# Performance work log

Measured on AMD Instinct MI355X. Metric: run time of the kernel, lower is better.

## Reference

```python
import jax, jax.numpy as jnp
import numpy as np

V, D, H, B, S, T, N_EXTRA = 32000, 256, 512, 16, 400, 100, 50


def _lstm_cell(x, h, c, Wih, Whh, b):
    g = x @ Wih.T + h @ Whh.T + b
    i, f, gg, o = jnp.split(g, 4, axis=-1)
    c = jax.nn.sigmoid(f) * c + jax.nn.sigmoid(i) * jnp.tanh(gg)
    h = jax.nn.sigmoid(o) * jnp.tanh(c)
    return h, c


def _run_lstm(xs, m, Wih, Whh, b):
    # xs: [S,B,D], m: [S,B,1] validity mask (packed-sequence semantics)
    Bz, Hh = xs.shape[1], Whh.shape[1]
    init = (jnp.zeros((Bz, Hh), xs.dtype), jnp.zeros((Bz, Hh), xs.dtype))
    def step(carry, inp):
        h, c = carry
        x, mm = inp
        hn, cn = _lstm_cell(x, h, c, Wih, Whh, b)
        h = jnp.where(mm, hn, h)
        c = jnp.where(mm, cn, c)
        return (h, c), jnp.where(mm, hn, 0.0)
    (h, c), ys = jax.lax.scan(step, init, (xs, m))
    return ys, h, c


def setup_inputs():
    key = jax.random.key(0)
    ks = jax.random.split(key, 20)
    def gn(k, shape, scale=0.05):
        return jax.random.normal(k, shape, dtype=jnp.float32) * scale
    inp = {}
    inp["source"] = jax.random.randint(ks[0], (B, S), 0, V)
    inp["source_extended"] = jax.random.randint(ks[1], (B, S), 0, V + N_EXTRA)
    inp["source_length"] = jax.random.randint(ks[2], (B,), S // 2, S + 1)
    inp["target"] = jax.random.randint(ks[3], (B, T), 0, V)
    inp["emb"] = gn(ks[4], (V, D), 0.1)
    inp["enc_Wih_f"] = gn(ks[5], (4 * H, D))
    inp["enc_Whh_f"] = gn(ks[6], (4 * H, H))
    inp["enc_b_f"] = jnp.zeros((4 * H,), jnp.float32)
    inp["enc_Wih_b"] = gn(ks[7], (4 * H, D))
    inp["enc_Whh_b"] = gn(ks[8], (4 * H, H))
    inp["enc_b_b"] = jnp.zeros((4 * H,), jnp.float32)
    inp["Wproj"] = gn(ks[9], (H, 2 * H))
    inp["bproj"] = jnp.zeros((H,), jnp.float32)
    inp["W2h"] = gn(ks[10], (H, 2 * H))
    inp["b2h"] = jnp.zeros((H,), jnp.float32)
    inp["W2c"] = gn(ks[11], (H, 2 * H))
    inp["b2c"] = jnp.zeros((H,), jnp.float32)
    inp["Wo1"] = gn(ks[12], (H, 2 * H))
    inp["bo1"] = jnp.zeros((H,), jnp.float32)
    inp["Wo2"] = gn(ks[13], (D, H))
    inp["dec_Wih"] = gn(ks[14], (4 * H, 2 * D))
    inp["dec_Whh"] = gn(ks[15], (4 * H, H))
    inp["dec_b"] = jnp.zeros((4 * H,), jnp.float32)
    inp["Wpgen"] = gn(ks[16], (1, 2 * H + 2 * D))
    inp["bpgen"] = jnp.zeros((1,), jnp.float32)
    return inp


def reference(source, source_extended, source_length, target, emb,
              enc_Wih_f, enc_Whh_f, enc_b_f, enc_Wih_b, enc_Whh_b, enc_b_b,
              Wproj, bproj, W2h, b2h, W2c, b2c, Wo1, bo1, Wo2,
              dec_Wih, dec_Whh, dec_b, Wpgen, bpgen):
    mask = jnp.arange(S)[None, :] < source_length[:, None]  # [B,S]
    w_s = emb[source]                                        # [B,S,D]
    xs = jnp.swapaxes(w_s, 0, 1)                             # [S,B,D]
    m = jnp.swapaxes(mask, 0, 1)[:, :, None]                 # [S,B,1]
    # bidirectional LSTM encoder
    ys_f, h_f, c_f = _run_lstm(xs, m, enc_Wih_f, enc_Whh_f, enc_b_f)
    ys_b, h_b, c_b = _run_lstm(xs[::-1], m[::-1], enc_Wih_b, enc_Whh_b, enc_b_b)
    ys_b = ys_b[::-1]
    enc_outs = jnp.swapaxes(jnp.concatenate([ys_f, ys_b], -1), 0, 1)  # [B,S,2H]
    enc_outs = enc_outs @ Wproj.T + bproj                             # [B,S,H]
    dec_h = jnp.concatenate([h_f, h_b], -1) @ W2h.T + b2h             # [B,H]
    dec_c = jnp.concatenate([c_f, c_b], -1) @ W2c.T + b2c             # [B,H]
    lens = source_length[:, None].astype(enc_outs.dtype)
    seq_mean = (enc_outs * mask[..., None]).sum(1) / lens             # [B,H]
    def out_proj(x):
        return jnp.tanh(x @ Wo1.T + bo1) @ Wo2.T
    dec_out0 = out_proj(jnp.concatenate([dec_h, seq_mean], -1))       # [B,D]
    neg = jnp.finfo(enc_outs.dtype).min
    extra = jnp.zeros((B, N_EXTRA), enc_outs.dtype)
    rows = jnp.arange(B)[:, None]
    w_t = jnp.swapaxes(emb[target], 0, 1)                             # [T,B,D]
    def step(carry, x_t):
        dec_out, h, c = carry
        x = jnp.concatenate([x_t, dec_out], -1)                       # [B,2D]
        h, c = _lstm_cell(x, h, c, dec_Wih, dec_Whh, dec_b)
        scores = jnp.einsum('bh,bsh->bs', h, enc_outs)
        attn = jax.nn.softmax(jnp.where(mask, scores, neg), axis=-1)  # point_dist
        context = jnp.einsum('bs,bsh->bh', attn, enc_outs)
        p_gen = jax.nn.sigmoid(jnp.concatenate([context, h, x], -1) @ Wpgen.T + bpgen)  # [B,1]
        dec_out = out_proj(jnp.concatenate([h, context], -1))         # [B,D]
        logit = dec_out @ emb.T                                       # [B,V]
        vocab_dist = jnp.concatenate([p_gen * jax.nn.softmax(logit, axis=-1), extra], -1)
        final = vocab_dist.at[rows, source_extended].add((1.0 - p_gen) * attn) + 1e-20
        return (dec_out, h, c), jnp.log(final)
    _, logits = jax.lax.scan(step, (dec_out0, dec_h, dec_c), w_t)
    return logits  # [T,B,V+N_EXTRA]
```

## Files before the change

### kernel.cpp

```cpp
#include <hip/hip_runtime.h>

#define V_SZ 32000
#define D_SZ 256
#define H_SZ 512
#define B_SZ 16
#define S_SZ 400
#define T_SZ 100
#define G4   2048
#define VX   32050
#define LINE 32

typedef unsigned short ushort_t;
typedef __attribute__((ext_vector_type(8))) __bf16 bf16x8;
typedef __attribute__((ext_vector_type(8))) unsigned short ushort8_t;
typedef __attribute__((ext_vector_type(4))) float f32x4;

__device__ __forceinline__ ushort_t f2bf(float x) {
  union { float f; unsigned u; } v; v.f = x;
  unsigned r = v.u + 0x7fffu + ((v.u >> 16) & 1u);
  return (ushort_t)(r >> 16);
}
__device__ __forceinline__ float bf2f(ushort_t x) {
  union { unsigned u; float f; } v; v.u = ((unsigned)x) << 16; return v.f;
}
__device__ __forceinline__ float bfu2f(unsigned x) {
  union { unsigned u; float f; } v; v.u = x << 16; return v.f;
}
__device__ __forceinline__ float sigf(float x) { return 1.0f / (1.0f + __expf(-x)); }
__device__ __forceinline__ float tanh_f(float x) {
  float e = __expf(2.0f * x);
  return 1.0f - 2.0f / (e + 1.0f);
}
__device__ __forceinline__ float dot4(f32x4 a, f32x4 b) {
  return a.x * b.x + a.y * b.y + a.z * b.z + a.w * b.w;
}
__device__ __forceinline__ void stg(float* p, float v) {
  __hip_atomic_store(p, v, __ATOMIC_RELAXED, __HIP_MEMORY_SCOPE_AGENT);
}
__device__ __forceinline__ void stg_u32(unsigned* p, unsigned v) {
  __hip_atomic_store(p, v, __ATOMIC_RELAXED, __HIP_MEMORY_SCOPE_AGENT);
}

__device__ __forceinline__ void slot_barrier(unsigned* slots, int myslot, int nslots,
                                             unsigned pc) {
  asm volatile("s_waitcnt vmcnt(0)" ::: "memory");
  __syncthreads();
  if (threadIdx.x == 0)
    __hip_atomic_store(&slots[myslot * LINE], pc, __ATOMIC_RELAXED, __HIP_MEMORY_SCOPE_AGENT);
  if (threadIdx.x < 64) {
    const int i0 = threadIdx.x, i1 = threadIdx.x + 64;
    for (;;) {
      unsigned v0 = pc, v1 = pc;
      if (i0 < nslots)
        v0 = __hip_atomic_load(&slots[i0 * LINE], __ATOMIC_RELAXED, __HIP_MEMORY_SCOPE_AGENT);
      if (i1 < nslots)
        v1 = __hip_atomic_load(&slots[i1 * LINE], __ATOMIC_RELAXED, __HIP_MEMORY_SCOPE_AGENT);
      if (__all((v0 >= pc) & (v1 >= pc))) break;
      __builtin_amdgcn_s_sleep(1);
    }
  }
  __syncthreads();
}

__global__ __launch_bounds__(256) void cvt_kernel(const float* in, ushort_t* outp, int n) {
  int i = blockIdx.x * 256 + threadIdx.x;
  int stride = gridDim.x * 256;
  for (; i < n; i += stride) outp[i] = f2bf(in[i]);
}

__global__ __launch_bounds__(256) void cvt_strided_kernel(const float* in, ushort_t* outp) {
  int gid = blockIdx.x * 256 + threadIdx.x;
  int r = gid >> 8, d = gid & 255;
  outp[gid] = f2bf(in[(size_t)r * 512 + d]);
}

__global__ __launch_bounds__(256) void cvt_wo2t_kernel(const float* wo2, ushort_t* outp) {
  int gid = blockIdx.x * 256 + threadIdx.x;
  int h = gid >> 8, d = gid & 255;
  outp[gid] = f2bf(wo2[(size_t)d * 512 + h]);
}

__global__ __launch_bounds__(256) void wfused_kernel(const float* dwih, const float* wo2,
                                                     float* wf) {
  __shared__ float xr_s[256];
  int r = blockIdx.x;
  xr_s[threadIdx.x] = dwih[(size_t)r * 512 + 256 + threadIdx.x];
  __syncthreads();
  float a0 = 0, a1 = 0;
  for (int d = 0; d < 256; ++d) {
    float x = xr_s[d];
    a0 += x * wo2[(size_t)d * 512 + threadIdx.x];
    a1 += x * wo2[(size_t)d * 512 + threadIdx.x + 256];
  }
  wf[(size_t)r * 512 + threadIdx.x] = a0;
  wf[(size_t)r * 512 + threadIdx.x + 256] = a1;
}

__global__ __launch_bounds__(256) void wfp_kernel(const float* wpgen, const float* wo2,
                                                  float* wfp) {
  int h = blockIdx.x * 256 + threadIdx.x;
  float a = 0;
  for (int d = 0; d < 256; ++d) a += wpgen[1280 + d] * wo2[(size_t)d * 512 + h];
  wfp[h] = a;
}

__global__ __launch_bounds__(256) void pack_whh_kernel(const float* whh_f, const float* whh_b,
                                                       ushort_t* outp) {
  int gid = blockIdx.x * 256 + threadIdx.x;
  int col = gid & 511;
  int p_g = gid >> 9;
  int dir = p_g >> 11, p = p_g & 2047;
  int ub = p >> 6, g = (p >> 4) & 3, u = p & 15;
  const float* src = dir ? whh_b : whh_f;
  outp[gid] = f2bf(src[(size_t)(g * 512 + ub * 16 + u) * 512 + col]);
}

__global__ __launch_bounds__(256) void pack_wdec_kernel(const float* dwhh, const float* wfused,
                                                        ushort_t* outp) {
  int gid = blockIdx.x * 256 + threadIdx.x;
  int col = gid & 1023;
  int p = gid >> 10;
  int ub = p >> 4, g = (p >> 2) & 3, u = p & 3;
  int row = g * 512 + ub * 4 + u;
  float v = (col < 512) ? dwhh[(size_t)row * 512 + col] : wfused[(size_t)row * 512 + (col - 512)];
  outp[gid] = f2bf(v);
}

__global__ __launch_bounds__(256) void gxT_kernel(const float* gx, float* gxT) {
  int t = blockIdx.y;
  int r = blockIdx.x * 256 + threadIdx.x;
  float v[16];
#pragma unroll
  for (int b = 0; b < 16; ++b) v[b] = gx[((size_t)t * 16 + b) * G4 + r];
  f32x4* dst = (f32x4*)(gxT + ((size_t)t * G4 + r) * 16);
#pragma unroll
  for (int q = 0; q < 4; ++q) {
    f32x4 w = {v[q * 4], v[q * 4 + 1], v[q * 4 + 2], v[q * 4 + 3]};
    dst[q] = w;
  }
}

__global__ __launch_bounds__(256) void gather_src_kernel(const ushort_t* emb_bf, const int* source,
                                                         ushort_t* xs_bf) {
  int gid = blockIdx.x * 256 + threadIdx.x;
  int r = gid >> 5, e = gid & 31;
  int s = r >> 4, b = r & 15;
  int tok = source[b * S_SZ + s];
  ((ushort8_t*)xs_bf)[gid] = ((const ushort8_t*)emb_bf)[(size_t)tok * 32 + e];
}
__global__ __launch_bounds__(256) void gather_tgt_kernel(const ushort_t* emb_bf, const int* target,
                                                         ushort_t* xt_bf) {
  int gid = blockIdx.x * 256 + threadIdx.x;
  int r = gid >> 5, e = gid & 31;
  int t = r >> 4, b = r & 15;
  int tok = target[b * T_SZ + t];
  ((ushort8_t*)xt_bf)[gid] = ((const ushort8_t*)emb_bf)[(size_t)tok * 32 + e];
}

__device__ __forceinline__ void mfma_16x64(const ushort_t* A, const ushort_t* B_, int K,
                                           int m0, int n0, f32x4 acc[4]) {
  const int lane = threadIdx.x & 63;
  const int lr = lane & 15, kh = lane >> 4;
  const ushort_t* ap = A + (size_t)(m0 + lr) * K + kh * 8;
  const ushort_t* bp = B_ + (size_t)(n0 + lr) * K + kh * 8;
  for (int k0 = 0; k0 < K; k0 += 32) {
    bf16x8 av = *(const bf16x8*)(ap + k0);
#pragma unroll
    for (int s = 0; s < 4; ++s) {
      bf16x8 bv = *(const bf16x8*)(bp + (size_t)s * 16 * K + k0);
      acc[s] = __builtin_amdgcn_mfma_f32_16x16x32_bf16(av, bv, acc[s], 0, 0, 0);
    }
  }
}

__global__ __launch_bounds__(256) void gemm_abt_bias(const ushort_t* A, const ushort_t* Bm,
                                                     const float* bias, float* out, int K) {
  int wave = threadIdx.x >> 6;
  int m0 = blockIdx.y * 16;
  int n0 = blockIdx.x * 256 + wave * 64;
  f32x4 acc[4] = {};
  mfma_16x64(A, Bm, K, m0, n0, acc);
  int lane = threadIdx.x & 63, lr = lane & 15, kh = lane >> 4;
#pragma unroll
  for (int s = 0; s < 4; ++s) {
    int n = n0 + s * 16 + lr;
    float bv = bias[n];
#pragma unroll
    for (int i = 0; i < 4; ++i) {
      int m = m0 + kh * 4 + i;
      out[(size_t)m * G4 + n] = acc[s][i] + bv;
    }
  }
}

__global__ __launch_bounds__(256) void gemm_encout(const ushort_t* ys_cat, const ushort_t* wproj_bf,
                                                   const float* bproj, float* enc_outs) {
  int wave = threadIdx.x >> 6;
  int m0 = blockIdx.y * 16;
  int n0 = blockIdx.x * 256 + wave * 64;
  f32x4 acc[4] = {};
  mfma_16x64(ys_cat, wproj_bf, 2 * H_SZ, m0, n0, acc);
  int lane = threadIdx.x & 63, lr = lane & 15, kh = lane >> 4;
#pragma unroll
  for (int s = 0; s < 4; ++s) {
    int n = n0 + s * 16 + lr;
    float bv = bproj[n];
#pragma unroll
    for (int i = 0; i < 4; ++i) {
      int m = m0 + kh * 4 + i;
      int b = m & 15, si = m >> 4;
      enc_outs[((size_t)b * S_SZ + si) * H_SZ + n] = acc[s][i] + bv;
    }
  }
}

__global__ __launch_bounds__(256) void gemm_e2(const ushort_t* emb_bf, const ushort_t* wo2t_bf,
                                               ushort_t* e2) {
  int wave = threadIdx.x >> 6;
  int m0 = blockIdx.y * 16;
  int n0 = blockIdx.x * 256 + wave * 64;
  f32x4 acc[4] = {};
  mfma_16x64(emb_bf, wo2t_bf, 256, m0, n0, acc);
  int lane = threadIdx.x & 63, lr = lane & 15, kh = lane >> 4;
#pragma unroll
  for (int s = 0; s < 4; ++s) {
    int n = n0 + s * 16 + lr;
#pragma unroll
    for (int i = 0; i < 4; ++i) {
      int m = m0 + kh * 4 + i;
      e2[(size_t)m * 512 + n] = f2bf(acc[s][i]);
    }
  }
}

__global__ __launch_bounds__(256) void gemm_logits(const ushort_t* tmp_bf, const ushort_t* e2_bf,
                                                   float* out) {
  int wave = threadIdx.x >> 6;
  int m0 = blockIdx.x * 16;
  int n0 = blockIdx.y * 256 + wave * 64;
  f32x4 acc[4] = {};
  mfma_16x64(tmp_bf, e2_bf, 512, m0, n0, acc);
  int lane = threadIdx.x & 63, lr = lane & 15, kh = lane >> 4;
#pragma unroll
  for (int s = 0; s < 4; ++s) {
    int n = n0 + s * 16 + lr;
#pragma unroll
    for (int i = 0; i < 4; ++i) {
      int m = m0 + kh * 4 + i;
      out[(size_t)m * VX + n] = acc[s][i];
    }
  }
}

__global__ __launch_bounds__(256) void enc_kernel(const float* gx_f, const float* gx_b,
                                                  const ushort_t* whh_pk, const int* src_len,
                                                  unsigned* hbf_f, unsigned* hbf_b,
                                                  unsigned* ys_cat_u32, float* h_final,
                                                  float* c_final, unsigned* ctrs) {
  __shared__ float gates_s[4 * 16 * 17];
  const int blk = blockIdx.x, tid = threadIdx.x;
  const int dir = blk >> 5, ub = blk & 31, j0 = ub * 16;
  const int g = tid >> 6, lane = tid & 63, lr = lane & 15, kh = lane >> 4;
  const float* gx = dir ? gx_b : gx_f;
  unsigned* hb = dir ? hbf_b : hbf_f;
  unsigned* slots = ctrs + dir * 1024;
  const ushort_t* wrow =
      whh_pk + (size_t)(((dir * 32 + ub) * 4 + g) * 16 + lr) * 512 + kh * 8;
  const int bc = tid >> 4, uc = tid & 15;
  const int len_b = src_len[bc];
  float c_reg = 0.0f, h_reg = 0.0f;

  int maxlen;
  {
    int v = src_len[lane & 15];
    v = max(v, __shfl_xor(v, 1));
    v = max(v, __shfl_xor(v, 2));
    v = max(v, __shfl_xor(v, 4));
    v = max(v, __shfl_xor(v, 8));
    maxlen = v;
  }
  for (int i = tid; i < (S_SZ - maxlen) * 128; i += 256) {
    int s = maxlen + (i >> 7);
    int r = i & 127;
    int bb = r >> 3, k = r & 7;
    ys_cat_u32[(size_t)(s * 16 + bb) * 512 + dir * 256 + (j0 >> 1) + k] = 0u;
  }

  float gxa[4];
  {
    const int s0 = dir ? (maxlen - 1) : 0;
    const float* g0 = gx + (size_t)s0 * (16 * 2048) + g * 512 + j0 + lr;
#pragma unroll
    for (int i = 0; i < 4; ++i) gxa[i] = g0[(size_t)(kh * 4 + i) * 2048];
  }

  for (int t = 0; t < maxlen; ++t) {
    const int s_pos = dir ? (maxlen - 1 - t) : t;
    float gxn[4] = {0.f, 0.f, 0.f, 0.f};
    if (t + 1 < maxlen) {
      const int sn = dir ? (maxlen - 2 - t) : (t + 1);
      const float* gn = gx + (size_t)sn * (16 * 2048) + g * 512 + j0 + lr;
#pragma unroll
      for (int i = 0; i < 4; ++i) gxn[i] = gn[(size_t)(kh * 4 + i) * 2048];
    }
    f32x4 acc = {0.f, 0.f, 0.f, 0.f};
    const ushort_t* ap = (const ushort_t*)(hb + (size_t)t * 4096) + lr * 512 + kh * 8;
#pragma unroll
    for (int k0 = 0; k0 < 512; k0 += 32)
      acc = __builtin_amdgcn_mfma_f32_16x16x32_bf16(*(const bf16x8*)(ap + k0),
                                                    *(const bf16x8*)(wrow + k0), acc, 0, 0, 0);
#pragma unroll
    for (int i = 0; i < 4; ++i)
      gates_s[(g * 16 + lr) * 17 + kh * 4 + i] = acc[i] + gxa[i];
    __syncthreads();
    float gi = gates_s[uc * 17 + bc];
    float gf = gates_s[(16 + uc) * 17 + bc];
    float gg = gates_s[(32 + uc) * 17 + bc];
    float go = gates_s[(48 + uc) * 17 + bc];
    bool msk = s_pos < len_b;
    float cn = sigf(gf) * c_reg + sigf(gi) * tanh_f(gg);
    float hn = sigf(go) * tanh_f(cn);
    float hout = msk ? hn : h_reg;
    if (msk) c_reg = cn;
    h_reg = hout;
    unsigned hbits = (unsigned)f2bf(hout);
    unsigned hpart = __shfl_xor(hbits, 1);
    unsigned ybits = msk ? (unsigned)f2bf(hn) : 0u;
    unsigned ypart = __shfl_xor(ybits, 1);
    if ((uc & 1) == 0) {
      stg_u32(&hb[(size_t)(t + 1) * 4096 + bc * 256 + ((j0 + uc) >> 1)], hbits | (hpart << 16));
      ys_cat_u32[(size_t)(s_pos * 16 + bc) * 512 + dir * 256 + ((j0 + uc) >> 1)] =
          ybits | (ypart << 16);
    }
    if (t == maxlen - 1) {
      h_final[dir * 8192 + bc * 512 + j0 + uc] = hout;
      c_final[dir * 8192 + bc * 512 + j0 + uc] = c_reg;
    }
    if (t + 1 < maxlen) slot_barrier(slots, ub, 32, (unsigned)(t + 1));
#pragma unroll
    for (int i = 0; i < 4; ++i) gxa[i] = gxn[i];
  }
}

__global__ __launch_bounds__(256) void seqmean_kernel(const float* enc_outs, const int* src_len,
                                                      float* seq_mean) {
  int b = blockIdx.x >> 1;
  int j = (blockIdx.x & 1) * 256 + threadIdx.x;
  int L = src_len[b];
  float a = 0;
  for (int s = 0; s < L; ++s) a += enc_outs[((size_t)b * S_SZ + s) * H_SZ + j];
  seq_mean[b * 512 + j] = a / (float)L;
}

__global__ __launch_bounds__(256) void init_state_kernel(const float* h_final, const float* c_final,
                                                         const float* w2h, const float* b2h,
                                                         const float* w2c, const float* b2c,
                                                         unsigned* h_u32, float* c_init) {
  int gid = blockIdx.x * 256 + threadIdx.x;
  int half = gid >> 13;
  int idx = gid & 8191;
  int b = idx >> 9, j = idx & 511;
  const float* src = half ? c_final : h_final;
  const float* w = (half ? w2c : w2h) + (size_t)j * 1024;
  float acc = (half ? b2c : b2h)[j];
  const f32x4* s0 = (const f32x4*)(src + b * 512);
  const f32x4* s1 = (const f32x4*)(src + 8192 + b * 512);
  const f32x4* w0 = (const f32x4*)w;
  const f32x4* w1 = w0 + 128;
  float a = 0;
  for (int k = 0; k < 128; ++k) a += dot4(s0[k], w0[k]);
  for (int k = 0; k < 128; ++k) a += dot4(s1[k], w1[k]);
  acc += a;
  if (half) {
    c_init[idx] = acc;
  } else {
    unsigned bits = (unsigned)f2bf(acc);
    unsigned pb2 = __shfl_xor(bits, 1);
    if ((j & 1) == 0) h_u32[b * 256 + (j >> 1)] = bits | (pb2 << 16);
  }
}

__global__ __launch_bounds__(256) void tmp0_kernel(const unsigned* h0_u32, const float* seq_mean,
                                                   const float* wo1, const float* bo1,
                                                   unsigned* tmp_u32) {
  int gid = blockIdx.x * 256 + threadIdx.x;
  int b = gid >> 9, j = gid & 511;
  const f32x4* x1 = (const f32x4*)(seq_mean + b * 512);
  const f32x4* w0 = (const f32x4*)(wo1 + (size_t)j * 1024);
  const f32x4* w1 = w0 + 128;
  float a = bo1[j];
  float p = 0;
  const ushort_t* h0 = (const ushort_t*)(h0_u32) + b * 512;
  for (int k = 0; k < 128; ++k) {
    f32x4 hv = {bf2f(h0[k * 4]), bf2f(h0[k * 4 + 1]), bf2f(h0[k * 4 + 2]), bf2f(h0[k * 4 + 3])};
    p += dot4(hv, w0[k]);
  }
  for (int k = 0; k < 128; ++k) p += dot4(x1[k], w1[k]);
  float tv = tanh_f(a + p);
  unsigned bits = (unsigned)f2bf(tv);
  unsigned pb2 = __shfl_xor(bits, 1);
  if ((j & 1) == 0) tmp_u32[b * 256 + (j >> 1)] = bits | (pb2 << 16);
}

__global__ __launch_bounds__(256) void dec_kernel(
    const ushort_t* xt_bf, const int* src_len, const ushort_t* wdec_pk,
    const float* wpgen, const float* bpgen, const float* wfp, const ushort_t* wo1_bf,
    const float* bo1, const float* enc_outs, const float* gxT, unsigned* h_u32,
    const float* c_init, unsigned* tmp_u32, float* ctx_part, float* z_part, float* zinv,
    float* pgen_o, float* pexp, unsigned* ctrs) {
  __shared__ ushort_t ec_s[50 * 512];
  __shared__ float part_s[4 * 16 * 17];
  __shared__ f32x4 smem4[272];
  __shared__ float red_s[8];
  __shared__ float p_s[64];
  float* sm = (float*)smem4;
  unsigned* gslots = ctrs + 2048;

  const int blk = blockIdx.x, tid = threadIdx.x;
  const int w = tid >> 6, lane = tid & 63, lr = lane & 15, kh = lane >> 4;
  const int j0 = blk * 4;
  const ushort_t* wrow = wdec_pk + (size_t)(blk * 16 + lr) * 1024 + w * 256 + kh * 8;
  const int b_c = (tid >> 2) & 15, u_c = tid & 3;
  float c_reg = (tid < 64) ? c_init[b_c * 512 + j0 + u_c] : 0.0f;
  const int b_pb = blk >> 3, ch = blk & 7, s0c = ch * 50;
  const int len_pb = src_len[b_pb];
  const int nc = ch;
  unsigned* grslots = ctrs + 8192 + b_pb * 256;
  unsigned gpc = 0;

  {
    const f32x4* ebase = (const f32x4*)(enc_outs + ((size_t)b_pb * S_SZ + s0c) * H_SZ);
    unsigned* dst = (unsigned*)ec_s;
    for (int i = tid; i < 6400; i += 256) {
      f32x4 v = ebase[i];
      dst[2 * i] = (unsigned)f2bf(v.x) | ((unsigned)f2bf(v.y) << 16);
      dst[2 * i + 1] = (unsigned)f2bf(v.z) | ((unsigned)f2bf(v.w) << 16);
    }
  }

  float gxa[4] = {0.f, 0.f, 0.f, 0.f};
  if (tid < 64) {
#pragma unroll
    for (int g2 = 0; g2 < 4; ++g2)
      gxa[g2] = gxT[((size_t)(g2 * 512 + j0 + u_c)) * 16 + b_c];
  }

  for (int t = 0; t < T_SZ; ++t) {
    {
      f32x4 acc = {0.f, 0.f, 0.f, 0.f};
      const unsigned* asrc = (w < 2) ? (h_u32 + (size_t)t * 4096) : (tmp_u32 + (size_t)t * 4096);
      const ushort_t* ap = (const ushort_t*)asrc + lr * 512 + (w & 1) * 256 + kh * 8;
#pragma unroll
      for (int k0 = 0; k0 < 256; k0 += 32)
        acc = __builtin_amdgcn_mfma_f32_16x16x32_bf16(*(const bf16x8*)(ap + k0),
                                                      *(const bf16x8*)(wrow + k0), acc, 0, 0, 0);
#pragma unroll
      for (int i = 0; i < 4; ++i) part_s[(w * 16 + lr) * 17 + kh * 4 + i] = acc[i];
      __syncthreads();
      if (tid < 64) {
        float gt[4];
#pragma unroll
        for (int g2 = 0; g2 < 4; ++g2) {
          int p = g2 * 4 + u_c;
          float a = gxa[g2];
#pragma unroll
          for (int w2 = 0; w2 < 4; ++w2) a += part_s[(w2 * 16 + p) * 17 + b_c];
          gt[g2] = a;
        }
        float cn = sigf(gt[1]) * c_reg + sigf(gt[0]) * tanh_f(gt[2]);
        c_reg = cn;
        float hn = sigf(gt[3]) * tanh_f(cn);
        unsigned bits = (unsigned)f2bf(hn);
        unsigned pb2 = __shfl_xor(bits, 1);
        if ((u_c & 1) == 0)
          stg_u32(&h_u32[(size_t)(t + 1) * 4096 + b_c * 256 + ((j0 + u_c) >> 1)],
                  bits | (pb2 << 16));
      }
    }
    slot_barrier(gslots, blk, 128, ++gpc);
    {
      if (tid < 64 && t + 1 < T_SZ) {
#pragma unroll
        for (int g2 = 0; g2 < 4; ++g2)
          gxa[g2] = gxT[((size_t)(t + 1) * G4 + g2 * 512 + j0 + u_c) * 16 + b_c];
      }
      if (tid < 128) {
        unsigned v0 = h_u32[(size_t)(t + 1) * 4096 + b_pb * 256 + tid * 2];
        unsigned v1 = h_u32[(size_t)(t + 1) * 4096 + b_pb * 256 + tid * 2 + 1];
        f32x4 hv = {bfu2f(v0 & 0xffffu), bfu2f(v0 >> 16), bfu2f(v1 & 0xffffu), bfu2f(v1 >> 16)};
        ((f32x4*)sm)[tid] = hv;
      }
      __syncthreads();
      int st = tid >> 2, kq = tid & 3;
      if (st < 50) {
        const ushort8_t* er = (const ushort8_t*)(ec_s + st * 512) + kq * 16;
        const f32x4* hr = (const f32x4*)sm + kq * 32;
        float sc = 0;
#pragma unroll 4
        for (int k = 0; k < 16; ++k) {
          ushort8_t w8 = er[k];
          f32x4 w0 = {bf2f(w8[0]), bf2f(w8[1]), bf2f(w8[2]), bf2f(w8[3])};
          f32x4 w1 = {bf2f(w8[4]), bf2f(w8[5]), bf2f(w8[6]), bf2f(w8[7])};
          sc += dot4(hr[2 * k], w0) + dot4(hr[2 * k + 1], w1);
        }
        sc += __shfl_xor(sc, 1);
        sc += __shfl_xor(sc, 2);
        if (kq == 0) {
          int s_abs = s0c + st;
          float p = (s_abs < len_pb) ? __expf(sc) : 0.0f;
          p_s[st] = p;
          pexp[((size_t)t * 16 + b_pb) * S_SZ + s_abs] = p;
        }
      }
      __syncthreads();
      if (tid == 0) {
        float z = 0;
        for (int s = 0; s < 50; ++s) z += p_s[s];
        stg(&z_part[((size_t)t * 16 + b_pb) * 8 + ch], z);
      }
      float a0 = 0, a1 = 0;
      for (int s = 0; s < 50; ++s) {
        float p = p_s[s];
        a0 += p * bf2f(ec_s[s * 512 + tid]);
        a1 += p * bf2f(ec_s[s * 512 + tid + 256]);
      }
      float* cp = ctx_part + (((size_t)t * 16 + b_pb) * 8 + ch) * 512;
      stg(&cp[tid], a0);
      stg(&cp[tid + 256], a1);
    }
    slot_barrier(grslots, ch, 8, (unsigned)(t + 1));
    {
      float* h_s = sm;
      float* ctx_s = sm + 512;
      const float* zp = z_part + ((size_t)t * 16 + b_pb) * 8;
      float z = 0;
#pragma unroll
      for (int c2 = 0; c2 < 8; ++c2) z += zp[c2];
      float inv = 1.0f / z;
      const float* cpb = ctx_part + ((size_t)t * 16 + b_pb) * 8 * 512;
      float c0 = 0, c1 = 0;
#pragma unroll
      for (int c2 = 0; c2 < 8; ++c2) {
        c0 += cpb[c2 * 512 + tid];
        c1 += cpb[c2 * 512 + tid + 256];
      }
      ctx_s[tid] = c0 * inv;
      ctx_s[tid + 256] = c1 * inv;
      __syncthreads();
      const ushort_t* tmpp = (const ushort_t*)(tmp_u32 + (size_t)t * 4096) + b_pb * 512;
      float tp0 = bf2f(tmpp[tid]);
      float tp1 = bf2f(tmpp[tid + 256]);
      float xe = bf2f(xt_bf[((size_t)t * 16 + b_pb) * 256 + tid]);
      float pg = wpgen[tid] * ctx_s[tid] + wpgen[tid + 256] * ctx_s[tid + 256] +
                 wpgen[512 + tid] * h_s[tid] + wpgen[512 + tid + 256] * h_s[tid + 256] +
                 wpgen[1024 + tid] * xe + wfp[tid] * tp0 + wfp[tid + 256] * tp1;
#pragma unroll
      for (int o = 32; o; o >>= 1) pg += __shfl_xor(pg, o);
      if (lane == 0) red_s[w] = pg;
      __syncthreads();
      if (nc == 0 && tid == 0) {
        pgen_o[t * 16 + b_pb] = sigf(red_s[0] + red_s[1] + red_s[2] + red_s[3] + bpgen[0]);
        zinv[t * 16 + b_pb] = inv;
      }
      int nidx = tid >> 2, kq = tid & 3;
      int n = nc * 64 + nidx;
      const ushort8_t* wrp = (const ushort8_t*)(wo1_bf + (size_t)n * 1024) + kq * 32;
      const f32x4* xr2 =
          (kq < 2) ? ((const f32x4*)h_s + kq * 64) : ((const f32x4*)ctx_s + (kq - 2) * 64);
      float a = 0;
#pragma unroll 4
      for (int k = 0; k < 32; ++k) {
        ushort8_t w8 = wrp[k];
        f32x4 w0 = {bf2f(w8[0]), bf2f(w8[1]), bf2f(w8[2]), bf2f(w8[3])};
        f32x4 w1 = {bf2f(w8[4]), bf2f(w8[5]), bf2f(w8[6]), bf2f(w8[7])};
        a += dot4(xr2[2 * k], w0) + dot4(xr2[2 * k + 1], w1);
      }
      a += __shfl_xor(a, 1);
      a += __shfl_xor(a, 2);
      float tv = tanh_f(a + bo1[n]);
      unsigned bits = (unsigned)f2bf(tv);
      unsigned pbits = __shfl_xor(bits, 4);
      if (kq == 0 && (nidx & 1) == 0)
        stg_u32(&tmp_u32[(size_t)(t + 1) * 4096 + b_pb * 256 + ((nc * 64 + nidx) >> 1)],
                bits | (pbits << 16));
    }
    if (t + 1 < T_SZ) slot_barrier(gslots, blk, 128, ++gpc);
  }
}

__global__ __launch_bounds__(1024) void finalize_kernel(float* out, const float* pexp,
                                                        const float* zinv, const float* pgen_i,
                                                        const int* src_ext) {
  __shared__ float scat[VX];
  __shared__ float red[64];
  const int row = blockIdx.x;
  const int b = row & 15;
  const int tid = threadIdx.x;
  for (int i = tid; i < VX; i += 1024) scat[i] = 0.0f;
  __syncthreads();
  const float pg = pgen_i[row];
  const float inv = zinv[row];
  if (tid < S_SZ) {
    float v = (1.0f - pg) * pexp[(size_t)row * S_SZ + tid] * inv;
    int col = src_ext[b * S_SZ + tid];
    atomicAdd(&scat[col], v);
  }
  float* orow = out + (size_t)row * VX;
  float l[32];
  float mx = -3.4e38f;
#pragma unroll
  for (int i2 = 0; i2 < 32; ++i2) {
    int col = tid + (i2 << 10);
    l[i2] = (col < V_SZ) ? orow[col] : -3.4e38f;
    mx = fmaxf(mx, l[i2]);
  }
#pragma unroll
  for (int o = 32; o; o >>= 1) mx = fmaxf(mx, __shfl_xor(mx, o));
  if ((tid & 63) == 0) red[16 + (tid >> 6)] = mx;
  __syncthreads();
  if (tid == 0) {
    float m2 = red[16];
    for (int w = 1; w < 16; ++w) m2 = fmaxf(m2, red[16 + w]);
    red[0] = m2;
  }
  __syncthreads();
  const float gmx = red[0];
  float se = 0.0f;
#pragma unroll
  for (int i2 = 0; i2 < 32; ++i2) {
    int col = tid + (i2 << 10);
    if (col < V_SZ) {
      l[i2] = __expf(l[i2] - gmx);
      se += l[i2];
    }
  }
#pragma unroll
  for (int o = 32; o; o >>= 1) se += __shfl_xor(se, o);
  if ((tid & 63) == 0) red[32 + (tid >> 6)] = se;
  __syncthreads();
  if (tid == 0) {
    float s2 = 0;
    for (int w = 0; w < 16; ++w) s2 += red[32 + w];
    red[1] = s2;
  }
  __syncthreads();
  const float scale = pg / red[1];
#pragma unroll
  for (int i2 = 0; i2 < 32; ++i2) {
    int col = tid + (i2 << 10);
    if (col < VX) {
      float base = (col < V_SZ) ? l[i2] * scale : 0.0f;
      orow[col] = __logf(base + scat[col] + 1e-20f);
    }
  }
}

extern "C" void kernel_launch(void* const* d_in, const int* in_sizes, int n_in, void* d_out,
                              int out_size, void* d_ws, size_t ws_size, hipStream_t stream) {
  (void)in_sizes; (void)n_in; (void)out_size; (void)ws_size;
  const int* source = (const int*)d_in[0];
  const int* source_ext = (const int*)d_in[1];
  const int* source_len = (const int*)d_in[2];
  const int* target = (const int*)d_in[3];
  const float* emb = (const float*)d_in[4];
  const float* wih_f = (const float*)d_in[5];
  const float* whh_f = (const float*)d_in[6];
  const float* b_f = (const float*)d_in[7];
  const float* wih_b = (const float*)d_in[8];
  const float* whh_b = (const float*)d_in[9];
  const float* b_b = (const float*)d_in[10];
  const float* wproj = (const float*)d_in[11];
  const float* bproj = (const float*)d_in[12];
  const float* w2h = (const float*)d_in[13];
  const float* b2h = (const float*)d_in[14];
  const float* w2c = (const float*)d_in[15];
  const float* b2c = (const float*)d_in[16];
  const float* wo1 = (const float*)d_in[17];
  const float* bo1 = (const float*)d_in[18];
  const float* wo2 = (const float*)d_in[19];
  const float* dwih = (const float*)d_in[20];
  const float* dwhh = (const float*)d_in[21];
  const float* dbias = (const float*)d_in[22];
  const float* wpgen = (const float*)d_in[23];
  const float* bpgen = (const float*)d_in[24];
  float* out = (float*)d_out;

  size_t off = 0;
  char* wsb = (char*)d_ws;
  auto alloc = [&](size_t bytes) -> void* {
    void* p = wsb + off;
    off += (bytes + 255) & ~(size_t)255;
    return p;
  };
  unsigned* ctrs = (unsigned*)alloc(64 * 1024);
  ushort_t* emb_bf = (ushort_t*)alloc((size_t)V_SZ * D_SZ * 2);
  ushort_t* wihf_bf = (ushort_t*)alloc((size_t)G4 * D_SZ * 2);
  ushort_t* wihb_bf = (ushort_t*)alloc((size_t)G4 * D_SZ * 2);
  ushort_t* wihd_bf = (ushort_t*)alloc((size_t)G4 * D_SZ * 2);
  ushort_t* wproj_bf = (ushort_t*)alloc((size_t)H_SZ * 2 * H_SZ * 2);
  ushort_t* wo2t_bf = (ushort_t*)alloc((size_t)H_SZ * D_SZ * 2);
  ushort_t* wo1_bf = (ushort_t*)alloc((size_t)H_SZ * 1024 * 2);
  float* wfused = (float*)alloc((size_t)G4 * H_SZ * 4);
  float* wfp = (float*)alloc(512 * 4);
  ushort_t* whh_pk = (ushort_t*)alloc((size_t)2 * G4 * H_SZ * 2);
  ushort_t* wdec_pk = (ushort_t*)alloc((size_t)G4 * 1024 * 2);
  ushort_t* xs_bf = (ushort_t*)alloc((size_t)S_SZ * B_SZ * D_SZ * 2);
  ushort_t* xt_bf = (ushort_t*)alloc((size_t)T_SZ * B_SZ * D_SZ * 2);
  float* gx_f = (float*)alloc((size_t)S_SZ * B_SZ * G4 * 4);
  float* gx_b = (float*)alloc((size_t)S_SZ * B_SZ * G4 * 4);
  unsigned* hbf_f = (unsigned*)alloc((size_t)(S_SZ + 1) * 4096 * 4);
  unsigned* hbf_b = (unsigned*)alloc((size_t)(S_SZ + 1) * 4096 * 4);
  unsigned* ys_cat_u32 = (unsigned*)alloc((size_t)S_SZ * B_SZ * 512 * 4);
  float* h_final = (float*)alloc((size_t)2 * B_SZ * H_SZ * 4);
  float* c_final = (float*)alloc((size_t)2 * B_SZ * H_SZ * 4);
  float* enc_outs = (float*)alloc((size_t)B_SZ * S_SZ * H_SZ * 4);
  float* seq_mean = (float*)alloc((size_t)B_SZ * H_SZ * 4);
  unsigned* h_u32 = (unsigned*)alloc((size_t)(T_SZ + 1) * 4096 * 4);
  float* c_init = (float*)alloc((size_t)B_SZ * H_SZ * 4);
  unsigned* tmp_u32 = (unsigned*)alloc((size_t)(T_SZ + 1) * 4096 * 4);
  float* z_part = (float*)alloc((size_t)T_SZ * B_SZ * 8 * 4);
  float* zinv = (float*)alloc((size_t)T_SZ * B_SZ * 4);
  float* pgen_b = (float*)alloc((size_t)T_SZ * B_SZ * 4);
  float* pexp = (float*)alloc((size_t)T_SZ * B_SZ * S_SZ * 4);
  ushort_t* e2_bf = (ushort_t*)gx_f;
  float* gx_dec = gx_b;
  float* ctx_part = gx_b + (size_t)3276800;
  float* gxT = gx_b + (size_t)9830400;

  hipMemsetAsync(ctrs, 0, 64 * 1024, stream);
  hipMemsetAsync(hbf_f, 0, 4096 * 4, stream);
  hipMemsetAsync(hbf_b, 0, 4096 * 4, stream);

  cvt_kernel<<<2048, 256, 0, stream>>>(emb, emb_bf, V_SZ * D_SZ);
  cvt_kernel<<<2048, 256, 0, stream>>>(wih_f, wihf_bf, G4 * D_SZ);
  cvt_kernel<<<2048, 256, 0, stream>>>(wih_b, wihb_bf, G4 * D_SZ);
  cvt_kernel<<<2048, 256, 0, stream>>>(wproj, wproj_bf, H_SZ * 2 * H_SZ);
  cvt_kernel<<<2048, 256, 0, stream>>>(wo1, wo1_bf, H_SZ * 1024);
  cvt_strided_kernel<<<2048, 256, 0, stream>>>(dwih, wihd_bf);
  cvt_wo2t_kernel<<<512, 256, 0, stream>>>(wo2, wo2t_bf);
  wfused_kernel<<<2048, 256, 0, stream>>>(dwih, wo2, wfused);
  wfp_kernel<<<2, 256, 0, stream>>>(wpgen, wo2, wfp);
  pack_whh_kernel<<<8192, 256, 0, stream>>>(whh_f, whh_b, whh_pk);
  pack_wdec_kernel<<<8192, 256, 0, stream>>>(dwhh, wfused, wdec_pk);
  gather_src_kernel<<<800, 256, 0, stream>>>(emb_bf, source, xs_bf);
  gather_tgt_kernel<<<200, 256, 0, stream>>>(emb_bf, target, xt_bf);
  gemm_abt_bias<<<dim3(8, 400), 256, 0, stream>>>(xs_bf, wihf_bf, b_f, gx_f, 256);
  gemm_abt_bias<<<dim3(8, 400), 256, 0, stream>>>(xs_bf, wihb_bf, b_b, gx_b, 256);
  enc_kernel<<<64, 256, 0, stream>>>(gx_f, gx_b, whh_pk, source_len, hbf_f, hbf_b, ys_cat_u32,
                                     h_final, c_final, ctrs);
  gemm_encout<<<dim3(2, 400), 256, 0, stream>>>((const ushort_t*)ys_cat_u32, wproj_bf, bproj,
                                                enc_outs);
  seqmean_kernel<<<32, 256, 0, stream>>>(enc_outs, source_len, seq_mean);
  init_state_kernel<<<64, 256, 0, stream>>>(h_final, c_final, w2h, b2h, w2c, b2c, h_u32, c_init);
  tmp0_kernel<<<32, 256, 0, stream>>>(h_u32, seq_mean, wo1, bo1, tmp_u32);
  gemm_abt_bias<<<dim3(8, 100), 256, 0, stream>>>(xt_bf, wihd_bf, dbias, gx_dec, 256);
  gxT_kernel<<<dim3(8, 100), 256, 0, stream>>>(gx_dec, gxT);
  gemm_e2<<<dim3(2, 2000), 256, 0, stream>>>(emb_bf, wo2t_bf, e2_bf);
  dec_kernel<<<128, 256, 0, stream>>>(xt_bf, source_len, wdec_pk, wpgen, bpgen, wfp, wo1_bf, bo1,
                                      enc_outs, gxT, h_u32, c_init, tmp_u32, ctx_part, z_part,
                                      zinv, pgen_b, pexp, ctrs);
  gemm_logits<<<dim3(100, 125), 256, 0, stream>>>((const ushort_t*)(tmp_u32 + 4096), e2_bf, out);
  finalize_kernel<<<1600, 1024, 0, stream>>>(out, pexp, zinv, pgen_b, source_ext);
}
```

Measured before the change: 4.863 ms.

## Overlap weight prep with encoder and stream logits GEMM alongside decoder

Moves the decoder weight conversions, packing, target gather and the emb·Wo2 GEMM into 192 extra blocks of the encoder kernel, so they run on idle CUs while the 64 recurrent blocks iterate. Also adds 128 extra blocks to the decoder kernel. One of them polls the tmp buffer (prefilled with a 0xFF sentinel) and raises a per-step tag, and the others compute each step's vocabulary logits GEMM as soon as that step is ready. This replaces a separate logits launch after the decoder. It risks contention with the latency-bound recurrent blocks, and correctness depends on co-residency and on the sentinel-based readiness scheme.

```diff
diff --git a/kernel.cpp b/kernel.cpp
--- a/kernel.cpp
+++ b/kernel.cpp
@@ -9,11 +9,13 @@
 #define G4   2048
 #define VX   32050
 #define LINE 32
+#define SENTU 0xFFFFFFFFu
 
 typedef unsigned short ushort_t;
 typedef __attribute__((ext_vector_type(8))) __bf16 bf16x8;
 typedef __attribute__((ext_vector_type(8))) unsigned short ushort8_t;
 typedef __attribute__((ext_vector_type(4))) float f32x4;
+typedef __attribute__((ext_vector_type(4))) unsigned u32x4;
 
 __device__ __forceinline__ ushort_t f2bf(float x) {
   union { float f; unsigned u; } v; v.f = x;
@@ -39,6 +41,18 @@
 }
 __device__ __forceinline__ void stg_u32(unsigned* p, unsigned v) {
   __hip_atomic_store(p, v, __ATOMIC_RELAXED, __HIP_MEMORY_SCOPE_AGENT);
+}
+__device__ __forceinline__ unsigned pollu(const unsigned* p) {
+  return __hip_atomic_load(p, __ATOMIC_RELAXED, __HIP_MEMORY_SCOPE_AGENT);
+}
+__device__ __forceinline__ unsigned okq(u32x4 c) {
+  return (unsigned)((c.x != SENTU) & (c.y != SENTU) & (c.z != SENTU) & (c.w != SENTU));
+}
+__device__ __forceinline__ u32x4 ld1_ic(const unsigned* p) {
+  u32x4 v;
+  asm volatile("global_load_dwordx4 %0, %1, off sc0 sc1\n\ts_waitcnt vmcnt(0)"
+               : "=&v"(v) : "v"(p) : "memory");
+  return v;
 }
 
 __device__ __forceinline__ void slot_barrier(unsigned* slots, int myslot, int nslots,
@@ -48,14 +62,13 @@
   if (threadIdx.x == 0)
     __hip_atomic_store(&slots[myslot * LINE], pc, __ATOMIC_RELAXED, __HIP_MEMORY_SCOPE_AGENT);
   if (threadIdx.x < 64) {
-    const int i0 = threadIdx.x, i1 = threadIdx.x + 64;
+    const int i0 = threadIdx.x, i1 = threadIdx.x + 64, i2 = threadIdx.x + 128;
     for (;;) {
-      unsigned v0 = pc, v1 = pc;
-      if (i0 < nslots)
-        v0 = __hip_atomic_load(&slots[i0 * LINE], __ATOMIC_RELAXED, __HIP_MEMORY_SCOPE_AGENT);
-      if (i1 < nslots)
-        v1 = __hip_atomic_load(&slots[i1 * LINE], __ATOMIC_RELAXED, __HIP_MEMORY_SCOPE_AGENT);
-      if (__all((v0 >= pc) & (v1 >= pc))) break;
+      unsigned v0 = pc, v1 = pc, v2 = pc;
+      if (i0 < nslots) v0 = pollu(&slots[i0 * LINE]);
+      if (i1 < nslots) v1 = pollu(&slots[i1 * LINE]);
+      if (i2 < nslots) v2 = pollu(&slots[i2 * LINE]);
+      if (__all((v0 >= pc) & (v1 >= pc) & (v2 >= pc))) break;
       __builtin_amdgcn_s_sleep(1);
     }
   }
@@ -66,42 +79,6 @@
   int i = blockIdx.x * 256 + threadIdx.x;
   int stride = gridDim.x * 256;
   for (; i < n; i += stride) outp[i] = f2bf(in[i]);
-}
-
-__global__ __launch_bounds__(256) void cvt_strided_kernel(const float* in, ushort_t* outp) {
-  int gid = blockIdx.x * 256 + threadIdx.x;
-  int r = gid >> 8, d = gid & 255;
-  outp[gid] = f2bf(in[(size_t)r * 512 + d]);
-}
-
-__global__ __launch_bounds__(256) void cvt_wo2t_kernel(const float* wo2, ushort_t* outp) {
-  int gid = blockIdx.x * 256 + threadIdx.x;
-  int h = gid >> 8, d = gid & 255;
-  outp[gid] = f2bf(wo2[(size_t)d * 512 + h]);
-}
-
-__global__ __launch_bounds__(256) void wfused_kernel(const float* dwih, const float* wo2,
-                                                     float* wf) {
-  __shared__ float xr_s[256];
-  int r = blockIdx.x;
-  xr_s[threadIdx.x] = dwih[(size_t)r * 512 + 256 + threadIdx.x];
-  __syncthreads();
-  float a0 = 0, a1 = 0;
-  for (int d = 0; d < 256; ++d) {
-    float x = xr_s[d];
-    a0 += x * wo2[(size_t)d * 512 + threadIdx.x];
-    a1 += x * wo2[(size_t)d * 512 + threadIdx.x + 256];
-  }
-  wf[(size_t)r * 512 + threadIdx.x] = a0;
-  wf[(size_t)r * 512 + threadIdx.x + 256] = a1;
-}
-
-__global__ __launch_bounds__(256) void wfp_kernel(const float* wpgen, const float* wo2,
-                                                  float* wfp) {
-  int h = blockIdx.x * 256 + threadIdx.x;
-  float a = 0;
-  for (int d = 0; d < 256; ++d) a += wpgen[1280 + d] * wo2[(size_t)d * 512 + h];
-  wfp[h] = a;
 }
 
 __global__ __launch_bounds__(256) void pack_whh_kernel(const float* whh_f, const float* whh_b,
@@ -115,17 +92,6 @@
   outp[gid] = f2bf(src[(size_t)(g * 512 + ub * 16 + u) * 512 + col]);
 }
 
-__global__ __launch_bounds__(256) void pack_wdec_kernel(const float* dwhh, const float* wfused,
-                                                        ushort_t* outp) {
-  int gid = blockIdx.x * 256 + threadIdx.x;
-  int col = gid & 1023;
-  int p = gid >> 10;
-  int ub = p >> 4, g = (p >> 2) & 3, u = p & 3;
-  int row = g * 512 + ub * 4 + u;
-  float v = (col < 512) ? dwhh[(size_t)row * 512 + col] : wfused[(size_t)row * 512 + (col - 512)];
-  outp[gid] = f2bf(v);
-}
-
 __global__ __launch_bounds__(256) void gxT_kernel(const float* gx, float* gxT) {
   int t = blockIdx.y;
   int r = blockIdx.x * 256 + threadIdx.x;
@@ -147,14 +113,6 @@
   int s = r >> 4, b = r & 15;
   int tok = source[b * S_SZ + s];
   ((ushort8_t*)xs_bf)[gid] = ((const ushort8_t*)emb_bf)[(size_t)tok * 32 + e];
-}
-__global__ __launch_bounds__(256) void gather_tgt_kernel(const ushort_t* emb_bf, const int* target,
-                                                         ushort_t* xt_bf) {
-  int gid = blockIdx.x * 256 + threadIdx.x;
-  int r = gid >> 5, e = gid & 31;
-  int t = r >> 4, b = r & 15;
-  int tok = target[b * T_SZ + t];
-  ((ushort8_t*)xt_bf)[gid] = ((const ushort8_t*)emb_bf)[(size_t)tok * 32 + e];
 }
 
 __device__ __forceinline__ void mfma_16x64(const ushort_t* A, const ushort_t* B_, int K,
@@ -214,51 +172,85 @@
   }
 }
 
-__global__ __launch_bounds__(256) void gemm_e2(const ushort_t* emb_bf, const ushort_t* wo2t_bf,
-                                               ushort_t* e2) {
-  int wave = threadIdx.x >> 6;
-  int m0 = blockIdx.y * 16;
-  int n0 = blockIdx.x * 256 + wave * 64;
-  f32x4 acc[4] = {};
-  mfma_16x64(emb_bf, wo2t_bf, 256, m0, n0, acc);
-  int lane = threadIdx.x & 63, lr = lane & 15, kh = lane >> 4;
-#pragma unroll
-  for (int s = 0; s < 4; ++s) {
-    int n = n0 + s * 16 + lr;
-#pragma unroll
-    for (int i = 0; i < 4; ++i) {
-      int m = m0 + kh * 4 + i;
-      e2[(size_t)m * 512 + n] = f2bf(acc[s][i]);
-    }
-  }
-}
-
-__global__ __launch_bounds__(256) void gemm_logits(const ushort_t* tmp_bf, const ushort_t* e2_bf,
-                                                   float* out) {
-  int wave = threadIdx.x >> 6;
-  int m0 = blockIdx.x * 16;
-  int n0 = blockIdx.y * 256 + wave * 64;
-  f32x4 acc[4] = {};
-  mfma_16x64(tmp_bf, e2_bf, 512, m0, n0, acc);
-  int lane = threadIdx.x & 63, lr = lane & 15, kh = lane >> 4;
-#pragma unroll
-  for (int s = 0; s < 4; ++s) {
-    int n = n0 + s * 16 + lr;
-#pragma unroll
-    for (int i = 0; i < 4; ++i) {
-      int m = m0 + kh * 4 + i;
-      out[(size_t)m * VX + n] = acc[s][i];
-    }
-  }
-}
-
-__global__ __launch_bounds__(256) void enc_kernel(const float* gx_f, const float* gx_b,
-                                                  const ushort_t* whh_pk, const int* src_len,
-                                                  unsigned* hbf_f, unsigned* hbf_b,
-                                                  unsigned* ys_cat_u32, float* h_final,
-                                                  float* c_final, unsigned* ctrs) {
+__global__ __launch_bounds__(256) void enc_kernel(
+    const float* gx_f, const float* gx_b, const ushort_t* whh_pk, const int* src_len,
+    unsigned* hbf_f, unsigned* hbf_b, unsigned* ys_cat_u32, float* h_final, float* c_final,
+    unsigned* ctrs,
+    const int* target, const ushort_t* emb_bf, ushort_t* xt_bf, const float* wo1,
+    ushort_t* wo1_bf, const float* dwih, ushort_t* wihd_bf, const float* wo2,
+    ushort_t* wo2t_bf, const float* wproj, ushort_t* wproj_bf, const float* wpgen, float* wfp,
+    float* wfused, const float* dwhh, ushort_t* wdec_pk, ushort_t* e2_bf) {
   __shared__ float gates_s[4 * 16 * 17];
+  __shared__ float xr_s[256];
   const int blk = blockIdx.x, tid = threadIdx.x;
+
+  if (blk >= 64) {
+    const int pid = blk - 64;
+    const int gtid = pid * 256 + tid;
+    const int GSTR = 192 * 256;
+    for (int i = gtid; i < 512 * 1024; i += GSTR) wo1_bf[i] = f2bf(wo1[i]);
+    for (int i = gtid; i < 2048 * 256; i += GSTR) {
+      int r = i >> 8, d = i & 255;
+      wihd_bf[i] = f2bf(dwih[(size_t)r * 512 + d]);
+    }
+    for (int i = gtid; i < 512 * 256; i += GSTR) {
+      int h2 = i >> 8, d2 = i & 255;
+      wo2t_bf[i] = f2bf(wo2[(size_t)d2 * 512 + h2]);
+    }
+    for (int i = gtid; i < 512 * 1024; i += GSTR) wproj_bf[i] = f2bf(wproj[i]);
+    for (int i = gtid; i < 51200; i += GSTR) {
+      int r = i >> 5, e = i & 31;
+      int tt = r >> 4, bb = r & 15;
+      int tok = target[bb * T_SZ + tt];
+      ((ushort8_t*)xt_bf)[i] = ((const ushort8_t*)emb_bf)[(size_t)tok * 32 + e];
+    }
+    for (int h2 = gtid; h2 < 512; h2 += GSTR) {
+      float a = 0;
+      for (int d = 0; d < 256; ++d) a += wpgen[1280 + d] * wo2[(size_t)d * 512 + h2];
+      wfp[h2] = a;
+    }
+    for (int r = pid; r < 2048; r += 192) {
+      xr_s[tid] = dwih[(size_t)r * 512 + 256 + tid];
+      __syncthreads();
+      float a0 = 0, a1 = 0;
+      for (int d = 0; d < 256; ++d) {
+        float x = xr_s[d];
+        a0 += x * wo2[(size_t)d * 512 + tid];
+        a1 += x * wo2[(size_t)d * 512 + tid + 256];
+      }
+      wfused[(size_t)r * 512 + tid] = a0;
+      wfused[(size_t)r * 512 + tid + 256] = a1;
+      __syncthreads();
+    }
+    slot_barrier(ctrs + 2048, pid, 192, 1u);
+    for (int i = gtid; i < 2048 * 1024; i += GSTR) {
+      int col = i & 1023, p = i >> 10;
+      int ub2 = p >> 4, g2 = (p >> 2) & 3, u2 = p & 3;
+      int row = g2 * 512 + ub2 * 4 + u2;
+      float v = (col < 512) ? dwhh[(size_t)row * 512 + col]
+                            : wfused[(size_t)row * 512 + (col - 512)];
+      wdec_pk[i] = f2bf(v);
+    }
+    for (int q = pid; q < 4000; q += 192) {
+      int mt = q >> 1, xt2 = q & 1;
+      int wave = tid >> 6;
+      int m0 = mt * 16, n0 = xt2 * 256 + wave * 64;
+      f32x4 acc[4] = {};
+      mfma_16x64(emb_bf, wo2t_bf, 256, m0, n0, acc);
+      int lane2 = tid & 63, lr2 = lane2 & 15, kh2 = lane2 >> 4;
+#pragma unroll
+      for (int s = 0; s < 4; ++s) {
+        int n = n0 + s * 16 + lr2;
+#pragma unroll
+        for (int i = 0; i < 4; ++i) {
+          int m = m0 + kh2 * 4 + i;
+          e2_bf[(size_t)m * 512 + n] = f2bf(acc[s][i]);
+        }
+      }
+    }
+    return;
+  }
+
   const int dir = blk >> 5, ub = blk & 31, j0 = ub * 16;
   const int g = tid >> 6, lane = tid & 63, lr = lane & 15, kh = lane >> 4;
   const float* gx = dir ? gx_b : gx_f;
@@ -407,16 +399,61 @@
     const float* wpgen, const float* bpgen, const float* wfp, const ushort_t* wo1_bf,
     const float* bo1, const float* enc_outs, const float* gxT, unsigned* h_u32,
     const float* c_init, unsigned* tmp_u32, float* ctx_part, float* z_part, float* zinv,
-    float* pgen_o, float* pexp, unsigned* ctrs) {
+    float* pgen_o, float* pexp, unsigned* ctrs, const ushort_t* e2_bf, float* out) {
   __shared__ ushort_t ec_s[50 * 512];
   __shared__ float part_s[4 * 16 * 17];
   __shared__ f32x4 smem4[272];
   __shared__ float red_s[8];
   __shared__ float p_s[64];
   float* sm = (float*)smem4;
-  unsigned* gslots = ctrs + 2048;
+  unsigned* gslots = ctrs + 8192;
 
   const int blk = blockIdx.x, tid = threadIdx.x;
+
+  if (blk >= 128) {
+    const int sp = blk - 128;
+    unsigned* tags = ctrs + 16384;
+    if (sp == 0) {
+      for (int t = 0; t < T_SZ; ++t) {
+        if (tid < 64) {
+          const unsigned* hp = tmp_u32 + (size_t)(t + 1) * 4096 + tid * 64;
+          for (;;) {
+            unsigned ok = 1;
+#pragma unroll
+            for (int k = 0; k < 16; ++k) ok &= okq(ld1_ic(hp + k * 4));
+            if (__all((int)ok)) break;
+            __builtin_amdgcn_s_sleep(8);
+          }
+          if (tid == 0) stg_u32(&tags[t * 32], 1u);
+        }
+        __syncthreads();
+      }
+    } else if (sp <= 125) {
+      const ushort_t* tmp_bf2 = (const ushort_t*)(tmp_u32 + 4096);
+      const int wave = tid >> 6;
+      const int n0 = (sp - 1) * 256 + wave * 64;
+      const int lane2 = tid & 63, lr2 = lane2 & 15, kh2 = lane2 >> 4;
+      for (int t = 0; t < T_SZ; ++t) {
+        if (tid < 64) {
+          while (pollu(&tags[t * 32]) == 0u) __builtin_amdgcn_s_sleep(4);
+        }
+        __syncthreads();
+        f32x4 acc[4] = {};
+        mfma_16x64(tmp_bf2, e2_bf, 512, t * 16, n0, acc);
+#pragma unroll
+        for (int s = 0; s < 4; ++s) {
+          int n = n0 + s * 16 + lr2;
+#pragma unroll
+          for (int i = 0; i < 4; ++i) {
+            int m = t * 16 + kh2 * 4 + i;
+            out[(size_t)m * VX + n] = acc[s][i];
+          }
+        }
+      }
+    }
+    return;
+  }
+
   const int w = tid >> 6, lane = tid & 63, lr = lane & 15, kh = lane >> 4;
   const int j0 = blk * 4;
   const ushort_t* wrow = wdec_pk + (size_t)(blk * 16 + lr) * 1024 + w * 256 + kh * 8;
@@ -425,7 +462,7 @@
   const int b_pb = blk >> 3, ch = blk & 7, s0c = ch * 50;
   const int len_pb = src_len[b_pb];
   const int nc = ch;
-  unsigned* grslots = ctrs + 8192 + b_pb * 256;
+  unsigned* grslots = ctrs + 12288 + b_pb * 256;
   unsigned gpc = 0;
 
   {
@@ -692,7 +729,7 @@
     off += (bytes + 255) & ~(size_t)255;
     return p;
   };
-  unsigned* ctrs = (unsigned*)alloc(64 * 1024);
+  unsigned* ctrs = (unsigned*)alloc(80 * 1024);
   ushort_t* emb_bf = (ushort_t*)alloc((size_t)V_SZ * D_SZ * 2);
   ushort_t* wihf_bf = (ushort_t*)alloc((size_t)G4 * D_SZ * 2);
   ushort_t* wihb_bf = (ushort_t*)alloc((size_t)G4 * D_SZ * 2);
@@ -706,6 +743,7 @@
   ushort_t* wdec_pk = (ushort_t*)alloc((size_t)G4 * 1024 * 2);
   ushort_t* xs_bf = (ushort_t*)alloc((size_t)S_SZ * B_SZ * D_SZ * 2);
   ushort_t* xt_bf = (ushort_t*)alloc((size_t)T_SZ * B_SZ * D_SZ * 2);
+  ushort_t* e2_bf = (ushort_t*)alloc((size_t)V_SZ * H_SZ * 2);
   float* gx_f = (float*)alloc((size_t)S_SZ * B_SZ * G4 * 4);
   float* gx_b = (float*)alloc((size_t)S_SZ * B_SZ * G4 * 4);
   unsigned* hbf_f = (unsigned*)alloc((size_t)(S_SZ + 1) * 4096 * 4);
@@ -722,32 +760,26 @@
   float* zinv = (float*)alloc((size_t)T_SZ * B_SZ * 4);
   float* pgen_b = (float*)alloc((size_t)T_SZ * B_SZ * 4);
   float* pexp = (float*)alloc((size_t)T_SZ * B_SZ * S_SZ * 4);
-  ushort_t* e2_bf = (ushort_t*)gx_f;
   float* gx_dec = gx_b;
   float* ctx_part = gx_b + (size_t)3276800;
   float* gxT = gx_b + (size_t)9830400;
 
-  hipMemsetAsync(ctrs, 0, 64 * 1024, stream);
+  hipMemsetAsync(ctrs, 0, 80 * 1024, stream);
+  hipMemsetAsync(tmp_u32, 0xFF, (size_t)(T_SZ + 1) * 4096 * 4, stream);
   hipMemsetAsync(hbf_f, 0, 4096 * 4, stream);
   hipMemsetAsync(hbf_b, 0, 4096 * 4, stream);
 
   cvt_kernel<<<2048, 256, 0, stream>>>(emb, emb_bf, V_SZ * D_SZ);
   cvt_kernel<<<2048, 256, 0, stream>>>(wih_f, wihf_bf, G4 * D_SZ);
   cvt_kernel<<<2048, 256, 0, stream>>>(wih_b, wihb_bf, G4 * D_SZ);
-  cvt_kernel<<<2048, 256, 0, stream>>>(wproj, wproj_bf, H_SZ * 2 * H_SZ);
-  cvt_kernel<<<2048, 256, 0, stream>>>(wo1, wo1_bf, H_SZ * 1024);
-  cvt_strided_kernel<<<2048, 256, 0, stream>>>(dwih, wihd_bf);
-  cvt_wo2t_kernel<<<512, 256, 0, stream>>>(wo2, wo2t_bf);
-  wfused_kernel<<<2048, 256, 0, stream>>>(dwih, wo2, wfused);
-  wfp_kernel<<<2, 256, 0, stream>>>(wpgen, wo2, wfp);
   pack_whh_kernel<<<8192, 256, 0, stream>>>(whh_f, whh_b, whh_pk);
-  pack_wdec_kernel<<<8192, 256, 0, stream>>>(dwhh, wfused, wdec_pk);
   gather_src_kernel<<<800, 256, 0, stream>>>(emb_bf, source, xs_bf);
-  gather_tgt_kernel<<<200, 256, 0, stream>>>(emb_bf, target, xt_bf);
   gemm_abt_bias<<<dim3(8, 400), 256, 0, stream>>>(xs_bf, wihf_bf, b_f, gx_f, 256);
   gemm_abt_bias<<<dim3(8, 400), 256, 0, stream>>>(xs_bf, wihb_bf, b_b, gx_b, 256);
-  enc_kernel<<<64, 256, 0, stream>>>(gx_f, gx_b, whh_pk, source_len, hbf_f, hbf_b, ys_cat_u32,
-                                     h_final, c_final, ctrs);
+  enc_kernel<<<256, 256, 0, stream>>>(gx_f, gx_b, whh_pk, source_len, hbf_f, hbf_b, ys_cat_u32,
+                                      h_final, c_final, ctrs, target, emb_bf, xt_bf, wo1, wo1_bf,
+                                      dwih, wihd_bf, wo2, wo2t_bf, wproj, wproj_bf, wpgen, wfp,
+                                      wfused, dwhh, wdec_pk, e2_bf);
   gemm_encout<<<dim3(2, 400), 256, 0, stream>>>((const ushort_t*)ys_cat_u32, wproj_bf, bproj,
                                                 enc_outs);
   seqmean_kernel<<<32, 256, 0, stream>>>(enc_outs, source_len, seq_mean);
@@ -755,10 +787,8 @@
   tmp0_kernel<<<32, 256, 0, stream>>>(h_u32, seq_mean, wo1, bo1, tmp_u32);
   gemm_abt_bias<<<dim3(8, 100), 256, 0, stream>>>(xt_bf, wihd_bf, dbias, gx_dec, 256);
   gxT_kernel<<<dim3(8, 100), 256, 0, stream>>>(gx_dec, gxT);
-  gemm_e2<<<dim3(2, 2000), 256, 0, stream>>>(emb_bf, wo2t_bf, e2_bf);
-  dec_kernel<<<128, 256, 0, stream>>>(xt_bf, source_len, wdec_pk, wpgen, bpgen, wfp, wo1_bf, bo1,
+  dec_kernel<<<256, 256, 0, stream>>>(xt_bf, source_len, wdec_pk, wpgen, bpgen, wfp, wo1_bf, bo1,
                                       enc_outs, gxT, h_u32, c_init, tmp_u32, ctx_part, z_part,
-                                      zinv, pgen_b, pexp, ctrs);
-  gemm_logits<<<dim3(100, 125), 256, 0, stream>>>((const ushort_t*)(tmp_u32 + 4096), e2_bf, out);
+                                      zinv, pgen_b, pexp, ctrs, e2_bf, out);
   finalize_kernel<<<1600, 1024, 0, stream>>>(out, pexp, zinv, pgen_b, source_ext);
 }
```

After: 4.317 ms. 1.13x faster.
